# Optimization experiments

Measured on AMD Instinct MI355X. Metric: run time of the kernel, lower is better.

Reference implementation:

```python
import jax, jax.numpy as jnp
import numpy as np

MARGIN = 0.3
EPS = 1e-6  # torch.nn.functional.pairwise_distance eps


def setup_inputs() -> dict:
    key = jax.random.key(0)
    k1, k2 = jax.random.split(key)
    B, D, C = 8192, 256, 512
    embeddings = jax.random.normal(k1, (B, D), dtype=jnp.float32)
    labels = jax.random.randint(k2, (B,), 0, C, dtype=jnp.int64)
    return {"embeddings": embeddings, "labels": labels}


def reference(embeddings, labels):
    B = embeddings.shape[0]
    # pairwise squared L2 via GEMM
    dot = embeddings @ embeddings.T                      # [B, B]
    sq = jnp.diag(dot)[:, None] + jnp.diag(dot)[None, :] - 2.0 * dot
    dist_sq = jnp.clip(sq, 0.0)

    same = labels[:, None] == labels[None, :]            # [B, B] bool
    eye = jnp.eye(B, dtype=bool)
    pos_mask = same & ~eye
    neg_mask = ~same

    valid = pos_mask.any(axis=1) & neg_mask.any(axis=1)  # [B]
    INF = dist_sq.max() + 1.0

    hardest_pos_idx = jnp.argmax(dist_sq * pos_mask.astype(dist_sq.dtype), axis=1)
    hardest_neg_idx = jnp.argmin(dist_sq + same.astype(dist_sq.dtype) * INF, axis=1)

    a = embeddings
    p = embeddings[hardest_pos_idx]
    n = embeddings[hardest_neg_idx]
    # torch pairwise_distance: ||x1 - x2 + eps||_2
    d_ap = jnp.linalg.norm(a - p + EPS, axis=1)
    d_an = jnp.linalg.norm(a - n + EPS, axis=1)
    per_anchor = jnp.maximum(d_ap - d_an + MARGIN, 0.0)

    v = valid.astype(per_anchor.dtype)
    n_valid = v.sum()
    loss = jnp.where(n_valid > 0, (per_anchor * v).sum() / jnp.maximum(n_valid, 1.0), 0.0)
    return loss
```

## Files before the change

kernel.cpp:

```cpp
#include <hip/hip_runtime.h>
#include <math.h>

#define NB 8192
#define ND 256
#define NSJ 8
#define JSLICE (NB / NSJ)
#define MARGIN_F 0.3f
#define EPS_F 1e-6f
#define BIAS_F 512.0f
#define NFIN 2048

typedef __attribute__((ext_vector_type(8))) short bf16x8;
typedef __attribute__((ext_vector_type(4))) float f32x4;

__device__ __forceinline__ unsigned short f2bf(float x) {
    unsigned int u = __float_as_uint(x);
    return (unsigned short)((u + 0x7fffu + ((u >> 16) & 1u)) >> 16);
}

__device__ __forceinline__ void gld16(const void* g, void* l) {
    __builtin_amdgcn_global_load_lds(
        (const __attribute__((address_space(1))) void*)g,
        (__attribute__((address_space(3))) void*)l, 16, 0, 0);
}

__global__ __launch_bounds__(512) void prep_k(const float* __restrict__ emb,
                                              unsigned short* __restrict__ ehi,
                                              float* __restrict__ sqnb,
                                              unsigned int* __restrict__ pos_key,
                                              unsigned int* __restrict__ neg_key) {
    __shared__ float sm[8][16];
    const int tid = threadIdx.x;
    const int tk = tid >> 6;
    const int lane = tid & 63;
    const int q = lane >> 4;
    const int lx = lane & 15;
    const int row = blockIdx.x * 16 + lx;
    const int k = tk * 32 + q * 8;

    const float4 v0 = *reinterpret_cast<const float4*>(&emb[(size_t)row * ND + k]);
    const float4 v1 = *reinterpret_cast<const float4*>(&emb[(size_t)row * ND + k + 4]);
    ushort4 h0, h1;
    h0.x = f2bf(v0.x); h0.y = f2bf(v0.y); h0.z = f2bf(v0.z); h0.w = f2bf(v0.w);
    h1.x = f2bf(v1.x); h1.y = f2bf(v1.y); h1.z = f2bf(v1.z); h1.w = f2bf(v1.w);
    *reinterpret_cast<ushort4*>(&ehi[(size_t)blockIdx.x * 4096 + tid * 8])     = h0;
    *reinterpret_cast<ushort4*>(&ehi[(size_t)blockIdx.x * 4096 + tid * 8 + 4]) = h1;

    if (tid >= 32 && tid < 48) pos_key[blockIdx.x * 16 + (tid - 32)] = 0u;
    if (tid >= 48 && tid < 64) neg_key[blockIdx.x * 16 + (tid - 48)] = 0xFFFFFFFFu;

    float s = v0.x * v0.x + v0.y * v0.y + v0.z * v0.z + v0.w * v0.w
            + v1.x * v1.x + v1.y * v1.y + v1.z * v1.z + v1.w * v1.w;
    s += __shfl_xor(s, 16, 64);
    s += __shfl_xor(s, 32, 64);
    if (q == 0) sm[tk][lx] = s;
    __syncthreads();
    if (tid < 16) {
        float t = 0.0f;
#pragma unroll
        for (int wv = 0; wv < 8; ++wv) t += sm[wv][tid];
        sqnb[blockIdx.x * 16 + tid] = t + BIAS_F;
    }
}

template <bool DIAG>
__device__ __forceinline__ void mine_tile(
        const f32x4 (&acc)[4][4], const float* __restrict__ sqj_s,
        const int* __restrict__ lbl_j_s, const int* __restrict__ lbl_i_s,
        int jb, unsigned (&pmax)[16], unsigned (&nmin)[16],
        int wr, int wc, int q, int lx) {
    int lblc[4]; float sqjc[4]; unsigned enc[4];
#pragma unroll
    for (int tc = 0; tc < 4; ++tc) {
        const int colb = wc + tc * 16 + lx;
        lblc[tc] = lbl_j_s[colb];
        sqjc[tc] = sqj_s[colb];
        enc[tc] = 8191u - (unsigned)(jb + colb);
    }
#pragma unroll
    for (int tr = 0; tr < 4; ++tr) {
#pragma unroll
        for (int reg = 0; reg < 4; ++reg) {
            const int r = tr * 4 + reg;
            const int rowb = wr + tr * 16 + q * 4 + reg;
            const int lab = lbl_i_s[rowb];
#pragma unroll
            for (int tc = 0; tc < 4; ++tc) {
                const float v = fmaf(-2.0f, acc[tr][tc][reg], sqjc[tc]);
                const unsigned key = (__float_as_uint(v) & 0xFFFFE000u) | enc[tc];
                const bool same = (lblc[tc] == lab);
                bool pc = same;
                if (DIAG) pc = same && ((wc + tc * 16 + lx) != rowb);
                const unsigned pk = pc ? key : 0u;
                const unsigned nk = same ? 0xFFFFFFFFu : key;
                pmax[r] = pmax[r] >= pk ? pmax[r] : pk;
                nmin[r] = nmin[r] <= nk ? nmin[r] : nk;
            }
        }
    }
}

__global__ __launch_bounds__(256, 2) void pair_k(
        const unsigned short* __restrict__ ehi, const float* __restrict__ sqnb,
        const int* __restrict__ labels,
        unsigned int* __restrict__ pos_key, unsigned int* __restrict__ neg_key) {
    __shared__ short Ash[8 * 512];
    __shared__ short Bsh[8 * 512];
    __shared__ int   lbl_i_s[128];
    __shared__ int   lbl_j_s[128];
    __shared__ float sqj_s[128];

    const int tid = threadIdx.x;
    const int w = tid >> 6;
    const int lane = tid & 63;
    const int q = lane >> 4;
    const int lx = lane & 15;
    const int i_base = blockIdx.x * 128;
    const int slice = blockIdx.y;
    const int wr = (w & 1) * 64;
    const int wc = (w >> 1) * 64;
    const int sa_base = (w & 1) * 4;
    const int sb_base = (w >> 1) * 4;
    const int ib16 = i_base >> 4;

    if (tid < 128) lbl_i_s[tid] = labels[i_base + tid];

    unsigned pmax[16], nmin[16];
#pragma unroll
    for (int r = 0; r < 16; ++r) { pmax[r] = 0u; nmin[r] = 0xFFFFFFFFu; }

#pragma unroll 1
    for (int jt = 0; jt < JSLICE / 128; ++jt) {
        const int jb = slice * JSLICE + jt * 128;
        const int jb16 = jb >> 4;
        __syncthreads();
        if (tid < 128)        sqj_s[tid] = sqnb[jb + tid];
        else                  lbl_j_s[tid - 128] = labels[jb + tid - 128];

        f32x4 acc[4][4];
#pragma unroll
        for (int a = 0; a < 4; ++a)
#pragma unroll
            for (int b = 0; b < 4; ++b) acc[a][b] = (f32x4){0.f, 0.f, 0.f, 0.f};

#pragma unroll 1
        for (int kb = 0; kb < 8; ++kb) {
            __syncthreads();
            {
                const int half = (w & 1) * 4;
                const int gb16 = (w < 2) ? ib16 : jb16;
                short* dst = (w < 2) ? Ash : Bsh;
#pragma unroll
                for (int m2 = 0; m2 < 4; ++m2) {
                    const int m = half + m2;
                    const unsigned short* g =
                        ehi + ((size_t)(gb16 + m) * 8 + kb) * 512 + lane * 8;
                    gld16(g, dst + m * 512);
                }
            }
            __syncthreads();

            bf16x8 ah[4], bh[4];
#pragma unroll
            for (int t = 0; t < 4; ++t) {
                ah[t] = *(const bf16x8*)&Ash[(sa_base + t) * 512 + lane * 8];
                bh[t] = *(const bf16x8*)&Bsh[(sb_base + t) * 512 + lane * 8];
            }
#pragma unroll
            for (int tr = 0; tr < 4; ++tr)
#pragma unroll
                for (int tc = 0; tc < 4; ++tc)
                    acc[tr][tc] = __builtin_amdgcn_mfma_f32_16x16x32_bf16(
                        ah[tr], bh[tc], acc[tr][tc], 0, 0, 0);
        }

        if (jb == i_base)
            mine_tile<true>(acc, sqj_s, lbl_j_s, lbl_i_s, jb, pmax, nmin, wr, wc, q, lx);
        else
            mine_tile<false>(acc, sqj_s, lbl_j_s, lbl_i_s, jb, pmax, nmin, wr, wc, q, lx);
    }

#pragma unroll
    for (int r = 0; r < 16; ++r) {
        unsigned pm = pmax[r], nm = nmin[r];
#pragma unroll
        for (int mm = 1; mm < 16; mm <<= 1) {
            const unsigned pm2 = __shfl_xor(pm, mm, 64);
            const unsigned nm2 = __shfl_xor(nm, mm, 64);
            pm = pm >= pm2 ? pm : pm2;
            nm = nm <= nm2 ? nm : nm2;
        }
        if (lx == r) {
            const int row = i_base + wr + (r >> 2) * 16 + q * 4 + (r & 3);
            atomicMax(&pos_key[row], pm);
            atomicMin(&neg_key[row], nm);
        }
    }
}

__global__ __launch_bounds__(256) void final_k(
        const float* __restrict__ emb,
        const unsigned int* __restrict__ pos_key, const unsigned int* __restrict__ neg_key,
        float* __restrict__ pbsum, float* __restrict__ pbcnt) {
    __shared__ float ssum[4], scnt[4];
    const int w = threadIdx.x >> 6;
    const int lane = threadIdx.x & 63;
    const int i = blockIdx.x * 4 + w;

    const unsigned pk = pos_key[i], nk = neg_key[i];
    const int pi = 8191 - (int)(pk & 8191u);
    const int ni = 8191 - (int)(nk & 8191u);
    const bool valid = (pk != 0u) && (nk != 0xFFFFFFFFu);

    const float4 av  = *reinterpret_cast<const float4*>(&emb[(size_t)i  * ND + lane * 4]);
    const float4 pvv = *reinterpret_cast<const float4*>(&emb[(size_t)pi * ND + lane * 4]);
    const float4 nvv = *reinterpret_cast<const float4*>(&emb[(size_t)ni * ND + lane * 4]);
    float sap, san;
    {
        const float d0 = av.x - pvv.x + EPS_F, d1 = av.y - pvv.y + EPS_F;
        const float d2 = av.z - pvv.z + EPS_F, d3 = av.w - pvv.w + EPS_F;
        sap = d0 * d0 + d1 * d1 + d2 * d2 + d3 * d3;
        const float e0 = av.x - nvv.x + EPS_F, e1 = av.y - nvv.y + EPS_F;
        const float e2 = av.z - nvv.z + EPS_F, e3 = av.w - nvv.w + EPS_F;
        san = e0 * e0 + e1 * e1 + e2 * e2 + e3 * e3;
    }
#pragma unroll
    for (int m = 32; m; m >>= 1) {
        sap += __shfl_down(sap, m, 64);
        san += __shfl_down(san, m, 64);
    }
    if (lane == 0) {
        const float per = fmaxf(sqrtf(sap) - sqrtf(san) + MARGIN_F, 0.0f);
        ssum[w] = valid ? per : 0.0f;
        scnt[w] = valid ? 1.0f : 0.0f;
    }
    __syncthreads();
    if (threadIdx.x == 0) {
        pbsum[blockIdx.x] = ssum[0] + ssum[1] + ssum[2] + ssum[3];
        pbcnt[blockIdx.x] = scnt[0] + scnt[1] + scnt[2] + scnt[3];
    }
}

__global__ __launch_bounds__(256) void reduce_k(const float* __restrict__ pbsum,
                                                const float* __restrict__ pbcnt,
                                                float* __restrict__ out) {
    __shared__ float fs[4], fc[4];
    const int tid = threadIdx.x;
    float s = 0.0f, c = 0.0f;
#pragma unroll
    for (int r = 0; r < NFIN / 256; ++r) {
        s += pbsum[r * 256 + tid];
        c += pbcnt[r * 256 + tid];
    }
#pragma unroll
    for (int m = 32; m; m >>= 1) { s += __shfl_down(s, m, 64); c += __shfl_down(c, m, 64); }
    const int wv = tid >> 6, lane = tid & 63;
    if (lane == 0) { fs[wv] = s; fc[wv] = c; }
    __syncthreads();
    if (tid == 0) {
        const float S = fs[0] + fs[1] + fs[2] + fs[3];
        const float C = fc[0] + fc[1] + fc[2] + fc[3];
        out[0] = (C > 0.0f) ? (S / fmaxf(C, 1.0f)) : 0.0f;
    }
}

extern "C" void kernel_launch(void* const* d_in, const int* in_sizes, int n_in,
                              void* d_out, int out_size, void* d_ws, size_t ws_size,
                              hipStream_t stream) {
    const float* emb = (const float*)d_in[0];
    const int* labels = (const int*)d_in[1];
    float* out = (float*)d_out;

    char* ws = (char*)d_ws;
    unsigned short* ehi = (unsigned short*)ws;
    float* sqnb = (float*)(ws + (size_t)NB * ND * 2);
    unsigned int* pos_key = (unsigned int*)(sqnb + NB);
    unsigned int* neg_key = pos_key + NB;
    float* pbsum = (float*)(neg_key + NB);
    float* pbcnt = pbsum + NFIN;

    hipLaunchKernelGGL(prep_k, dim3(NB / 16), dim3(512), 0, stream,
                       emb, ehi, sqnb, pos_key, neg_key);
    hipLaunchKernelGGL(pair_k, dim3(NB / 128, NSJ), dim3(256), 0, stream,
                       ehi, sqnb, labels, pos_key, neg_key);
    hipLaunchKernelGGL(final_k, dim3(NFIN), dim3(256), 0, stream,
                       emb, pos_key, neg_key, pbsum, pbcnt);
    hipLaunchKernelGGL(reduce_k, dim3(1), dim3(256), 0, stream, pbsum, pbcnt, out);
}
```

Before: 128.4 us.

## Keep A tile in registers and stage full-K B tile in LDS

The anchor-row A fragments for all K blocks are loaded once into registers per block and reused across every j tile, so A no longer goes through LDS on each tile. For each j tile, the whole 128xK B slab (64 KB) is fetched into LDS in one pass, replacing eight per-K-block load/sync rounds with one barrier pair and a fully unrolled K loop. This cuts barrier count and redundant A traffic. In exchange it uses much more LDS (64 KB) and adds 128 VGPRs for A, which may lower occupancy below the launch bound of 2 blocks and may cause spills.

```diff
diff --git a/kernel.cpp b/kernel.cpp
--- a/kernel.cpp
+++ b/kernel.cpp
@@ -104,8 +104,7 @@
         const unsigned short* __restrict__ ehi, const float* __restrict__ sqnb,
         const int* __restrict__ labels,
         unsigned int* __restrict__ pos_key, unsigned int* __restrict__ neg_key) {
-    __shared__ short Ash[8 * 512];
-    __shared__ short Bsh[8 * 512];
+    __shared__ short Bsh[64 * 512];
     __shared__ int   lbl_i_s[128];
     __shared__ int   lbl_j_s[128];
     __shared__ float sqj_s[128];
@@ -119,11 +118,17 @@
     const int slice = blockIdx.y;
     const int wr = (w & 1) * 64;
     const int wc = (w >> 1) * 64;
-    const int sa_base = (w & 1) * 4;
-    const int sb_base = (w >> 1) * 4;
     const int ib16 = i_base >> 4;
 
     if (tid < 128) lbl_i_s[tid] = labels[i_base + tid];
+
+    bf16x8 areg[4][8];
+#pragma unroll
+    for (int t = 0; t < 4; ++t)
+#pragma unroll
+        for (int kb = 0; kb < 8; ++kb)
+            areg[t][kb] = *(const bf16x8*)&ehi[
+                ((size_t)(ib16 + (w & 1) * 4 + t) * 8 + kb) * 512 + lane * 8];
 
     unsigned pmax[16], nmin[16];
 #pragma unroll
@@ -132,10 +137,16 @@
 #pragma unroll 1
     for (int jt = 0; jt < JSLICE / 128; ++jt) {
         const int jb = slice * JSLICE + jt * 128;
-        const int jb16 = jb >> 4;
         __syncthreads();
+        {
+            const unsigned short* srcB = ehi + (size_t)(jb >> 4) * 4096;
+#pragma unroll
+            for (int p = 0; p < 16; ++p)
+                gld16(srcB + ((size_t)p * 256 + tid) * 8, Bsh + (p * 256 + tid) * 8);
+        }
         if (tid < 128)        sqj_s[tid] = sqnb[jb + tid];
         else                  lbl_j_s[tid - 128] = labels[jb + tid - 128];
+        __syncthreads();
 
         f32x4 acc[4][4];
 #pragma unroll
@@ -143,35 +154,20 @@
 #pragma unroll
             for (int b = 0; b < 4; ++b) acc[a][b] = (f32x4){0.f, 0.f, 0.f, 0.f};
 
-#pragma unroll 1
+#pragma unroll
         for (int kb = 0; kb < 8; ++kb) {
-            __syncthreads();
-            {
-                const int half = (w & 1) * 4;
-                const int gb16 = (w < 2) ? ib16 : jb16;
-                short* dst = (w < 2) ? Ash : Bsh;
-#pragma unroll
-                for (int m2 = 0; m2 < 4; ++m2) {
-                    const int m = half + m2;
-                    const unsigned short* g =
-                        ehi + ((size_t)(gb16 + m) * 8 + kb) * 512 + lane * 8;
-                    gld16(g, dst + m * 512);
-                }
-            }
-            __syncthreads();
-
-            bf16x8 ah[4], bh[4];
-#pragma unroll
-            for (int t = 0; t < 4; ++t) {
-                ah[t] = *(const bf16x8*)&Ash[(sa_base + t) * 512 + lane * 8];
-                bh[t] = *(const bf16x8*)&Bsh[(sb_base + t) * 512 + lane * 8];
+            bf16x8 bh[4];
+#pragma unroll
+            for (int tc = 0; tc < 4; ++tc) {
+                const int cs = (w >> 1) * 4 + tc;
+                bh[tc] = *(const bf16x8*)&Bsh[(cs * 8 + kb) * 512 + lane * 8];
             }
 #pragma unroll
             for (int tr = 0; tr < 4; ++tr)
 #pragma unroll
                 for (int tc = 0; tc < 4; ++tc)
                     acc[tr][tc] = __builtin_amdgcn_mfma_f32_16x16x32_bf16(
-                        ah[tr], bh[tc], acc[tr][tc], 0, 0, 0);
+                        areg[tr][kb], bh[tc], acc[tr][tc], 0, 0, 0);
         }
 
         if (jb == i_base)
```

After: 139.9 us. 9.0% more time.
